# Performance work log

Hardware: AMD Instinct MI355X
Metric: run time of the kernel (lower is better)

The kernel has to match this reference:

```python
import jax, jax.numpy as jnp
import numpy as np

B = 1024        # batch
C = 256         # channels (nodes)
ORDER = 4       # power-series order
DIM = C * (C - 1) // 2  # number of node pairs (edges)
LEAKY_SLOPE = 0.01      # torch nn.LeakyReLU default


def _diff_matrix():
    # column e corresponds to pair (p, q), p < q: diff = x_p - x_q
    p, q = np.triu_indices(C, k=1)
    D = np.zeros((C, DIM), dtype=np.float32)
    e = np.arange(DIM)
    D[p, e] = 1.0
    D[q, e] = -1.0
    return jnp.asarray(D)


def setup_inputs() -> dict:
    key = jax.random.key(0)
    k1, k2 = jax.random.split(key, 2)
    x = jax.random.normal(k1, (B, C), dtype=jnp.float32)
    w1 = jnp.ones((C,), dtype=jnp.float32)            # DiagonalLinear init: zeros + 1
    w2 = jax.random.normal(k2, (ORDER,), dtype=jnp.float32) * 0.1  # Grandson_net Linear(order,1) weight
    w3 = jnp.ones((DIM,), dtype=jnp.float32)          # DiagonalLinear on dim
    return {"x": x, "w1": w1, "w2": w2, "w3": w3, "diff_indices": _diff_matrix()}


def reference(x, w1, w2, w3, diff_indices):
    # fc1: diagonal scaling (the original wastes a full matmul on diag_embed)
    o1 = x * w1                                   # [B, C]
    diffs = o1 @ diff_indices                     # [B, DIM] pairwise differences
    sign = jnp.sign(diffs)
    a = jnp.abs(diffs)
    # power series a^1 .. a^ORDER (original stacks then loops Grandson_net per dim;
    # the Linear(order,1) is shared, so it is a single contraction over ORDER)
    pows = jnp.stack([a ** (i + 1) for i in range(ORDER)], axis=2)  # [B, DIM, ORDER]
    o3 = jax.nn.leaky_relu(jnp.einsum('bdo,o->bd', pows, w2), LEAKY_SLOPE)
    o3 = o3 * sign * w3                           # restore sign, fc3 diagonal scale
    # node aggregation: out[:, i] = -sum_{e: i is + end} o3[:, e] + sum_{e: i is - end} o3[:, e]
    # which is exactly -o3 @ diff_indices^T
    out = -(o3 @ diff_indices.T)                  # [B, C]
    return out[..., None]                         # [B, C, 1]
```

## Files before the change

kernel.cpp:

```cpp
#include <hip/hip_runtime.h>


#define C_NODES 256
#define BT      64
#define NW      8

__global__ __launch_bounds__(512, 4) void son_kernel(
    const float* __restrict__ x, const float* __restrict__ w1,
    const float* __restrict__ w2, const float* __restrict__ w3,
    float* __restrict__ out)
{
    __shared__ __align__(16) float o1t[BT * C_NODES];
    __shared__ __align__(16) float wrow[NW * C_NODES];

    const int t  = threadIdx.x;
    const int b0 = blockIdx.x * BT;

    {
        const int chunk = t & 63;
        const int c4    = chunk << 2;
        const float4 w1v = *(const float4*)&w1[c4];
        #pragma unroll
        for (int p = 0; p < 8; ++p) {
            const int row = (t >> 6) + (p << 3);
            const float4 xv = *(const float4*)&x[(b0 + row) * C_NODES + c4];
            float4 o;
            o.x = xv.x * w1v.x; o.y = xv.y * w1v.y;
            o.z = xv.z * w1v.z; o.w = xv.w * w1v.w;
            const int phys = chunk ^ (row & 7);
            *(float4*)&o1t[(row << 8) + (phys << 2)] = o;
        }
    }

    {
        const int lane = t & 63;
        const int wv_  = t >> 6;
        const int i    = blockIdx.y * NW + wv_;
        float4 wv;
        #pragma unroll
        for (int k = 0; k < 4; ++k) {
            const int j = lane * 4 + k;
            const int p = (i < j) ? i : j;
            const int q = (i < j) ? j : i;
            ((float*)&wv)[k] = (i == j) ? 0.f
                             : -w3[(p * (511 - p)) / 2 + q - p - 1];
        }
        *(float4*)&wrow[(wv_ << 8) + (lane << 2)] = wv;
    }
    __syncthreads();

    const int lane    = t & 63;
    const int w       = __builtin_amdgcn_readfirstlane(t >> 6);
    const int i       = blockIdx.y * NW + w;
    const int swz     = lane & 7;
    const int rowbase = lane << 8;

    const float c0 = w2[0], c1 = w2[1], c2 = w2[2], c3 = w2[3];

    const float oi = o1t[rowbase + ((((i >> 2) ^ swz) << 2) | (i & 3))];

    float acc = 0.f;

    #pragma unroll 8
    for (int jc = 0; jc < 64; ++jc) {
        const float4 ov = *(const float4*)&o1t[rowbase + ((jc ^ swz) << 2)];
        const float4 wa = *(const float4*)&wrow[(w << 8) + (jc << 2)];
        #pragma unroll
        for (int k = 0; k < 4; ++k) {
            const float oj  = ((const float*)&ov)[k];
            const float d   = oi - oj;
            const float a   = fabsf(d);
            const float t3  = __builtin_fmaf(a, __builtin_fmaf(a,
                                __builtin_fmaf(a, c3, c2), c1), c0);
            const float t3s = fmaxf(t3, 0.01f * t3);
            acc = __builtin_fmaf(d * t3s, ((const float*)&wa)[k], acc);
        }
    }

    out[(b0 + lane) * C_NODES + i] = acc;
}

extern "C" void kernel_launch(void* const* d_in, const int* in_sizes, int n_in,
                              void* d_out, int out_size, void* d_ws, size_t ws_size,
                              hipStream_t stream) {
    const float* x  = (const float*)d_in[0];
    const float* w1 = (const float*)d_in[1];
    const float* w2 = (const float*)d_in[2];
    const float* w3 = (const float*)d_in[3];
    float* out = (float*)d_out;

    const int B = in_sizes[0] / C_NODES;
    dim3 grid(B / BT, C_NODES / NW);
    son_kernel<<<grid, 512, 0, stream>>>(x, w1, w2, w3, out);
}
```

Measured before the change: 19.27 us.

## Precompute dense edge-weight matrix in separate kernel and split accumulator chains

```diff
diff --git a/kernel.cpp b/kernel.cpp
--- a/kernel.cpp
+++ b/kernel.cpp
@@ -5,13 +5,23 @@
 #define BT      64
 #define NW      8
 
+__global__ __launch_bounds__(256) void build_W(const float* __restrict__ w3,
+                                               float* __restrict__ W)
+{
+    const int i = blockIdx.x;
+    const int j = threadIdx.x;
+    const int p = (i < j) ? i : j;
+    const int q = (i < j) ? j : i;
+    W[(i << 8) + j] = (i == j) ? 0.f
+                    : -w3[(p * (511 - p)) / 2 + q - p - 1];
+}
+
 __global__ __launch_bounds__(512, 4) void son_kernel(
     const float* __restrict__ x, const float* __restrict__ w1,
-    const float* __restrict__ w2, const float* __restrict__ w3,
+    const float* __restrict__ w2, const float* __restrict__ W,
     float* __restrict__ out)
 {
     __shared__ __align__(16) float o1t[BT * C_NODES];
-    __shared__ __align__(16) float wrow[NW * C_NODES];
 
     const int t  = threadIdx.x;
     const int b0 = blockIdx.x * BT;
@@ -31,22 +41,6 @@
             *(float4*)&o1t[(row << 8) + (phys << 2)] = o;
         }
     }
-
-    {
-        const int lane = t & 63;
-        const int wv_  = t >> 6;
-        const int i    = blockIdx.y * NW + wv_;
-        float4 wv;
-        #pragma unroll
-        for (int k = 0; k < 4; ++k) {
-            const int j = lane * 4 + k;
-            const int p = (i < j) ? i : j;
-            const int q = (i < j) ? j : i;
-            ((float*)&wv)[k] = (i == j) ? 0.f
-                             : -w3[(p * (511 - p)) / 2 + q - p - 1];
-        }
-        *(float4*)&wrow[(wv_ << 8) + (lane << 2)] = wv;
-    }
     __syncthreads();
 
     const int lane    = t & 63;
@@ -56,28 +50,39 @@
     const int rowbase = lane << 8;
 
     const float c0 = w2[0], c1 = w2[1], c2 = w2[2], c3 = w2[3];
+    const float* __restrict__ Wrow = W + (i << 8);
 
     const float oi = o1t[rowbase + ((((i >> 2) ^ swz) << 2) | (i & 3))];
 
-    float acc = 0.f;
+    float acc0 = 0.f, acc1 = 0.f, acc2 = 0.f, acc3 = 0.f;
 
     #pragma unroll 8
     for (int jc = 0; jc < 64; ++jc) {
         const float4 ov = *(const float4*)&o1t[rowbase + ((jc ^ swz) << 2)];
-        const float4 wa = *(const float4*)&wrow[(w << 8) + (jc << 2)];
-        #pragma unroll
-        for (int k = 0; k < 4; ++k) {
-            const float oj  = ((const float*)&ov)[k];
-            const float d   = oi - oj;
-            const float a   = fabsf(d);
-            const float t3  = __builtin_fmaf(a, __builtin_fmaf(a,
-                                __builtin_fmaf(a, c3, c2), c1), c0);
-            const float t3s = fmaxf(t3, 0.01f * t3);
-            acc = __builtin_fmaf(d * t3s, ((const float*)&wa)[k], acc);
-        }
+        const float w0 = Wrow[4 * jc + 0];
+        const float w1s = Wrow[4 * jc + 1];
+        const float w2s = Wrow[4 * jc + 2];
+        const float w3s = Wrow[4 * jc + 3];
+
+        {   const float d = oi - ov.x, a = fabsf(d);
+            const float t3 = __builtin_fmaf(a, __builtin_fmaf(a,
+                               __builtin_fmaf(a, c3, c2), c1), c0);
+            acc0 = __builtin_fmaf(d * fmaxf(t3, 0.01f * t3), w0, acc0); }
+        {   const float d = oi - ov.y, a = fabsf(d);
+            const float t3 = __builtin_fmaf(a, __builtin_fmaf(a,
+                               __builtin_fmaf(a, c3, c2), c1), c0);
+            acc1 = __builtin_fmaf(d * fmaxf(t3, 0.01f * t3), w1s, acc1); }
+        {   const float d = oi - ov.z, a = fabsf(d);
+            const float t3 = __builtin_fmaf(a, __builtin_fmaf(a,
+                               __builtin_fmaf(a, c3, c2), c1), c0);
+            acc2 = __builtin_fmaf(d * fmaxf(t3, 0.01f * t3), w2s, acc2); }
+        {   const float d = oi - ov.w, a = fabsf(d);
+            const float t3 = __builtin_fmaf(a, __builtin_fmaf(a,
+                               __builtin_fmaf(a, c3, c2), c1), c0);
+            acc3 = __builtin_fmaf(d * fmaxf(t3, 0.01f * t3), w3s, acc3); }
     }
 
-    out[(b0 + lane) * C_NODES + i] = acc;
+    out[(b0 + lane) * C_NODES + i] = (acc0 + acc1) + (acc2 + acc3);
 }
 
 extern "C" void kernel_launch(void* const* d_in, const int* in_sizes, int n_in,
@@ -88,8 +93,11 @@
     const float* w2 = (const float*)d_in[2];
     const float* w3 = (const float*)d_in[3];
     float* out = (float*)d_out;
+    float* W   = (float*)d_ws;
+
+    build_W<<<C_NODES, C_NODES, 0, stream>>>(w3, W);
 
     const int B = in_sizes[0] / C_NODES;
     dim3 grid(B / BT, C_NODES / NW);
-    son_kernel<<<grid, 512, 0, stream>>>(x, w1, w2, w3, out);
+    son_kernel<<<grid, 512, 0, stream>>>(x, w1, w2, W, out);
 }
```

After: 26.47 us. 37.4% more time.
